# Kernel optimization log

Measured on AMD Instinct MI355X. Metric: run time of the kernel, lower is better.

Reference implementation:

```python
import jax, jax.numpy as jnp
import numpy as np

EPS = 1e-5

def conv1x1(x, W, b):
    # x: [B,C,H,W], W: [O,C], b: [O] -- a 1x1 conv is a per-pixel matmul
    return jnp.einsum('bchw,oc->bohw', x, W) + b[None, :, None, None]

def mean_variance_norm(feat):
    # torch .var(dim=2) is unbiased (ddof=1)
    m = feat.mean(axis=(2, 3), keepdims=True)
    v = feat.var(axis=(2, 3), ddof=1, keepdims=True)
    return (feat - m) / jnp.sqrt(v + EPS)

def setup_inputs() -> dict:
    key = jax.random.key(0)
    ks = jax.random.split(key, 10)
    B, C, H, W = 4, 256, 64, 64
    sc = 1.0 / np.sqrt(C)
    return {
        'content': jax.random.normal(ks[0], (B, C, H, W), jnp.float32),
        'style': jax.random.normal(ks[1], (B, C, H, W), jnp.float32),
        'content_key': jax.random.normal(ks[2], (B, C, H, W), jnp.float32),
        'style_key': jax.random.normal(ks[3], (B, C, H, W), jnp.float32),
        'Wf': jax.random.normal(ks[4], (C, C), jnp.float32) * sc,
        'bf': jnp.zeros((C,), jnp.float32),
        'Wg': jax.random.normal(ks[5], (C, C), jnp.float32) * sc,
        'bg': jnp.zeros((C,), jnp.float32),
        'Wh': jax.random.normal(ks[6], (C, C), jnp.float32) * sc,
        'bh': jnp.zeros((C,), jnp.float32),
    }

def reference(content, style, content_key, style_key, Wf, bf, Wg, bg, Wh, bh):
    Fq = conv1x1(content_key, Wf, bf)   # [B,Ck,H,W]
    G = conv1x1(style_key, Wg, bg)      # [B,Ck,Hs,Ws]
    Hv = conv1x1(style, Wh, bh)         # [B,C,Hs,Ws]
    b, _, h, w = Fq.shape
    _, C, hs, ws = Hv.shape
    N, M = h * w, hs * ws
    q = Fq.reshape(b, -1, N).transpose(0, 2, 1)   # [B,N,Ck]
    k = G.reshape(b, -1, M)                        # [B,Ck,M]
    style_flat = Hv.reshape(b, C, M).transpose(0, 2, 1)  # [B,M,C]
    # masks are all-ones -> attn_mask all zeros -> no masking (faithful to None path)
    S = jax.nn.softmax(jnp.einsum('bnc,bcm->bnm', q, k), axis=-1)  # [B,N,M]
    mean = jnp.einsum('bnm,bmc->bnc', S, style_flat)               # [B,N,C]
    std = jnp.sqrt(jax.nn.relu(
        jnp.einsum('bnm,bmc->bnc', S, style_flat * style_flat) - mean * mean))
    mean = mean.reshape(b, h, w, C).transpose(0, 3, 1, 2)  # [B,C,H,W]
    std = std.reshape(b, h, w, C).transpose(0, 3, 1, 2)
    return std * mean_variance_norm(content) + mean
```

## Files before the change

### kernel.cpp

```cpp
#include <hip/hip_runtime.h>


typedef unsigned int u32;
typedef unsigned short u16;
typedef _Float16 f16x8 __attribute__((ext_vector_type(8)));
typedef float f32x4 __attribute__((ext_vector_type(4)));
typedef float f32x16 __attribute__((ext_vector_type(16)));

#define L2E 1.44269504088896340736f
#define MFMA(a, b, c) __builtin_amdgcn_mfma_f32_16x16x32_f16(a, b, c, 0, 0, 0)
#define MFMA32(a, b, c) __builtin_amdgcn_mfma_f32_32x32x16_f16(a, b, c, 0, 0, 0)
#define EXP2(x) __builtin_amdgcn_exp2f(x)

__device__ __forceinline__ u16 h_bits(_Float16 h) { return __builtin_bit_cast(u16, h); }
__device__ __forceinline__ u16 f2h(float f) { return h_bits((_Float16)f); }

__device__ __forceinline__ f16x8 ldh8(const u16* p) {
    uint4 v = *(const uint4*)p;
    return __builtin_bit_cast(f16x8, v);
}

__global__ void k_stats(const float* __restrict__ content,
                        float* __restrict__ cm, float* __restrict__ cr) {
    int blk = blockIdx.x;
    const float* p = content + (size_t)blk * 4096;
    int t = threadIdx.x;
    float s = 0.f, ss = 0.f;
    for (int i = 0; i < 4; i++) {
        float4 v = *(const float4*)(p + (i * 256 + t) * 4);
        s  += (v.x + v.y) + (v.z + v.w);
        ss += (v.x * v.x + v.y * v.y) + (v.z * v.z + v.w * v.w);
    }
    for (int d = 32; d >= 1; d >>= 1) { s += __shfl_xor(s, d); ss += __shfl_xor(ss, d); }
    __shared__ __align__(16) float as[4], ass[4];
    int w = t >> 6;
    if ((t & 63) == 0) { as[w] = s; ass[w] = ss; }
    __syncthreads();
    if (t == 0) {
        s  = (as[0] + as[1]) + (as[2] + as[3]);
        ss = (ass[0] + ass[1]) + (ass[2] + ass[3]);
        float mean = s * (1.0f / 4096.0f);
        float var = (ss - s * mean) * (1.0f / 4095.0f);
        cm[blk] = mean;
        cr[blk] = rsqrtf(var + 1e-5f);
    }
}

__global__ void k_prep(const float* __restrict__ style, const float* __restrict__ ckey,
                       const float* __restrict__ skey,
                       const float* __restrict__ Wf, const float* __restrict__ Wg,
                       const float* __restrict__ Wh,
                       u16* __restrict__ X1, u16* __restrict__ X2, u16* __restrict__ Cc,
                       u16* __restrict__ Wb) {
    int z = blockIdx.z, t = threadIdx.x;
    if (z >= 12) {
        if (blockIdx.y != 0) return;
        int m = z - 12;
        const float* src = (m == 0) ? Wf : ((m == 1) ? Wg : Wh);
        u16* dst = Wb + m * 65536;
        int i = (blockIdx.x * 256 + t) * 4;
        float4 v = *(const float4*)(src + i);
        ushort4 o;
        o.x = f2h(v.x); o.y = f2h(v.y); o.z = f2h(v.z); o.w = f2h(v.w);
        *(ushort4*)(dst + i) = o;
        return;
    }
    int tensor = z >> 2, b = z & 3;
    const float* src = ((tensor == 0) ? style : ((tensor == 1) ? ckey : skey))
                       + (size_t)b * 256 * 4096;
    u16* dst = ((tensor == 0) ? X1 : ((tensor == 1) ? X2 : Cc)) + (size_t)b * 4096 * 256;
    int c0 = blockIdx.y * 64, t0 = blockIdx.x * 64;
    __shared__ __align__(16) float ls[64][65];
    int tr = t >> 4, tc = t & 15;
    for (int i = 0; i < 4; i++) {
        int c_off = i * 16 + tr;
        float4 v = *(const float4*)(src + (size_t)(c0 + c_off) * 4096 + t0 + tc * 4);
        ls[tc * 4 + 0][c_off] = v.x;
        ls[tc * 4 + 1][c_off] = v.y;
        ls[tc * 4 + 2][c_off] = v.z;
        ls[tc * 4 + 3][c_off] = v.w;
    }
    __syncthreads();
    for (int i = 0; i < 4; i++) {
        int tokrow = i * 16 + tr;
        ushort4 o;
        o.x = f2h(ls[tokrow][tc * 4 + 0]);
        o.y = f2h(ls[tokrow][tc * 4 + 1]);
        o.z = f2h(ls[tokrow][tc * 4 + 2]);
        o.w = f2h(ls[tokrow][tc * 4 + 3]);
        *(ushort4*)(dst + (size_t)(t0 + tokrow) * 256 + c0 + tc * 4) = o;
    }
}

__launch_bounds__(256, 2)
__global__ void k_gemm(const u16* X1, const u16* X2, u16* Cc,
                       u16* A, u16* Bv, const u16* __restrict__ Wb,
                       const float* __restrict__ bfp, const float* __restrict__ bgp,
                       const float* __restrict__ bhp) {
    int mode = blockIdx.z, b = blockIdx.y, tok0 = blockIdx.x * 128;
    const u16* X = ((mode == 0) ? X2 : ((mode == 1) ? (const u16*)Cc : X1))
                   + (size_t)b * 4096 * 256;
    const u16* W = Wb + mode * 65536;
    const float* bias = (mode == 0) ? bfp : ((mode == 1) ? bgp : bhp);
    __shared__ __align__(16) u16 wt[256 * 40];
    int t = threadIdx.x, w = t >> 6, lane = t & 63, ln = lane & 15, quad = lane >> 4;

    f32x4 acc[8][4];
    for (int i = 0; i < 8; i++)
        for (int j = 0; j < 4; j++) acc[i][j] = f32x4{0.f, 0.f, 0.f, 0.f};

    for (int ks = 0; ks < 8; ks++) {
        {
            const u16* wr = W + t * 256 + ks * 32;
            uint4 w0 = *(const uint4*)(wr + 0);
            uint4 w1 = *(const uint4*)(wr + 8);
            uint4 w2 = *(const uint4*)(wr + 16);
            uint4 w3 = *(const uint4*)(wr + 24);
            *(uint4*)(wt + t * 40 + 0)  = w0;
            *(uint4*)(wt + t * 40 + 8)  = w1;
            *(uint4*)(wt + t * 40 + 16) = w2;
            *(uint4*)(wt + t * 40 + 24) = w3;
        }
        __syncthreads();
        f16x8 wf[4];
        #pragma unroll
        for (int ct = 0; ct < 4; ct++)
            wf[ct] = ldh8(wt + (w * 64 + ct * 16 + ln) * 40 + quad * 8);
        #pragma unroll
        for (int rt = 0; rt < 8; rt++) {
            f16x8 xf = ldh8(X + (size_t)(tok0 + rt * 16 + ln) * 256 + ks * 32 + quad * 8);
            if (mode < 2) {
                #pragma unroll
                for (int ct = 0; ct < 4; ct++) acc[rt][ct] = MFMA(xf, wf[ct], acc[rt][ct]);
            } else {
                #pragma unroll
                for (int ct = 0; ct < 4; ct++) acc[rt][ct] = MFMA(wf[ct], xf, acc[rt][ct]);
            }
        }
        __syncthreads();
    }

    if (mode < 2) {
        u16* O = ((mode == 0) ? A : Cc) + (size_t)b * 4096 * 256;
        float bv[4];
        #pragma unroll
        for (int ct = 0; ct < 4; ct++) bv[ct] = bias[w * 64 + ct * 16 + ln];
        #pragma unroll
        for (int rt = 0; rt < 8; rt++)
            #pragma unroll
            for (int ct = 0; ct < 4; ct++)
                #pragma unroll
                for (int r = 0; r < 4; r++) {
                    int tok = tok0 + rt * 16 + quad * 4 + r;
                    int o = w * 64 + ct * 16 + ln;
                    O[(size_t)tok * 256 + o] = f2h(acc[rt][ct][r] + bv[ct]);
                }
    } else {
        u16* OV = Bv + (size_t)b * 256 * 4096;
        #pragma unroll
        for (int ct = 0; ct < 4; ct++)
            #pragma unroll
            for (int r = 0; r < 4; r++) {
                int o = w * 64 + ct * 16 + quad * 4 + r;
                float bb = bias[o];
                #pragma unroll
                for (int rt = 0; rt < 8; rt++) {
                    int tok = tok0 + rt * 16 + ln;
                    OV[(size_t)o * 4096 + tok] = f2h(acc[rt][ct][r] + bb);
                }
            }
    }
}

__launch_bounds__(256, 2)
__global__ void k_flash(const u16* __restrict__ Qt, const u16* __restrict__ Kt,
                        const u16* __restrict__ Vt,
                        const float* __restrict__ content, const float* __restrict__ cm,
                        const float* __restrict__ cr, float* __restrict__ out) {
    __shared__ __align__(16) char smem[67584];
    u16* Ks = (u16*)smem;
    u16* Vs = (u16*)(smem + 33792);
    int t = threadIdx.x, w = t >> 6, l = t & 63, lq = l & 31, h = l >> 5;
    u16* Psw = (u16*)(smem + 43008) + w * 2304;

    int b = blockIdx.y, q0 = blockIdx.x * 128, coff = blockIdx.z * 64;

    f16x8 qf[16];
    {
        const u16* qp = Qt + ((size_t)b * 4096 + q0 + w * 32 + lq) * 256 + h * 8;
        #pragma unroll
        for (int ks = 0; ks < 16; ks++) qf[ks] = ldh8(qp + ks * 16);
    }

    f32x16 am[2], aq[2];
    #pragma unroll
    for (int i = 0; i < 16; i++) { am[0][i] = 0.f; am[1][i] = 0.f; aq[0][i] = 0.f; aq[1][i] = 0.f; }
    float mrow = -1e30f, lrow = 0.f;

    const u16* Kg = Kt + (size_t)b * 4096 * 256;
    const u16* Vg = Vt + ((size_t)b * 256 + coff) * 4096;

    for (int it = 0; it < 64; it++) {
        int m0 = it * 64;
        #pragma unroll
        for (int i = 0; i < 8; i++) {
            int e = i * 256 + t, row = e >> 5, c16 = e & 31;
            *(uint4*)(Ks + row * 264 + c16 * 8) =
                *(const uint4*)(Kg + (size_t)(m0 + row) * 256 + c16 * 8);
        }
        #pragma unroll
        for (int i = 0; i < 2; i++) {
            int e = i * 256 + t, row = e >> 3, m16 = e & 7;
            *(uint4*)(Vs + row * 72 + m16 * 8) =
                *(const uint4*)(Vg + (size_t)row * 4096 + m0 + m16 * 8);
        }
        __syncthreads();

        f32x16 s0, s1;
        #pragma unroll
        for (int i = 0; i < 16; i++) { s0[i] = 0.f; s1[i] = 0.f; }
        #pragma unroll
        for (int ks = 0; ks < 16; ks++) {
            f16x8 k0 = ldh8(Ks + lq * 264 + ks * 16 + h * 8);
            s0 = MFMA32(k0, qf[ks], s0);
            f16x8 k1 = ldh8(Ks + (32 + lq) * 264 + ks * 16 + h * 8);
            s1 = MFMA32(k1, qf[ks], s1);
        }

        float mt = s0[0];
        #pragma unroll
        for (int r = 1; r < 16; r++) mt = fmaxf(mt, s0[r]);
        #pragma unroll
        for (int r = 0; r < 16; r++) mt = fmaxf(mt, s1[r]);
        mt = fmaxf(mt, __shfl_xor(mt, 32));
        float mn = fmaxf(mrow, mt);
        float al = EXP2((mrow - mn) * L2E);
        mrow = mn;
        float base = mn * L2E;
        float rs = 0.f;
        #pragma unroll
        for (int r = 0; r < 16; r++) {
            float p0 = (float)(_Float16)EXP2(__builtin_fmaf(s0[r], L2E, -base));
            float p1 = (float)(_Float16)EXP2(__builtin_fmaf(s1[r], L2E, -base));
            s0[r] = p0; s1[r] = p1;
            rs += p0 + p1;
        }
        rs += __shfl_xor(rs, 32);
        lrow = lrow * al + rs;

        #pragma unroll
        for (int r = 0; r < 16; r++) {
            float sc = __shfl(al, 8 * (r >> 2) + 4 * h + (r & 3));
            am[0][r] *= sc; am[1][r] *= sc;
            aq[0][r] *= sc; aq[1][r] *= sc;
        }

        #pragma unroll
        for (int mt2 = 0; mt2 < 2; mt2++)
            #pragma unroll
            for (int rq = 0; rq < 4; rq++) {
                float e0 = mt2 ? s1[4 * rq + 0] : s0[4 * rq + 0];
                float e1 = mt2 ? s1[4 * rq + 1] : s0[4 * rq + 1];
                float e2 = mt2 ? s1[4 * rq + 2] : s0[4 * rq + 2];
                float e3 = mt2 ? s1[4 * rq + 3] : s0[4 * rq + 3];
                uint2 pk;
                pk.x = (u32)f2h(e0) | ((u32)f2h(e1) << 16);
                pk.y = (u32)f2h(e2) | ((u32)f2h(e3) << 16);
                *(uint2*)(Psw + lq * 72 + mt2 * 32 + rq * 8 + h * 4) = pk;
            }

        #pragma unroll
        for (int ks = 0; ks < 4; ks++) {
            f16x8 pf = ldh8(Psw + lq * 72 + ks * 16 + h * 8);
            #pragma unroll
            for (int ct = 0; ct < 2; ct++) {
                f16x8 vf = ldh8(Vs + (ct * 32 + lq) * 72 + ks * 16 + h * 8);
                am[ct] = MFMA32(pf, vf, am[ct]);
                f16x8 vh = vf * vf;
                f16x8 vl = __builtin_elementwise_fma(vf, vf, -vh);
                aq[ct] = MFMA32(pf, vh, aq[ct]);
                aq[ct] = MFMA32(pf, vl, aq[ct]);
            }
        }
        __syncthreads();
    }

    float inv = 1.0f / lrow;
    float iv[16];
    #pragma unroll
    for (int r = 0; r < 16; r++) iv[r] = __shfl(inv, (r & 3) + 8 * (r >> 2) + 4 * h);
    float* Ms = (float*)smem;
    float* Ss = (float*)(smem + 33792);
    #pragma unroll
    for (int ct = 0; ct < 2; ct++)
        #pragma unroll
        for (int rq = 0; rq < 4; rq++) {
            f32x4 mv, sv;
            #pragma unroll
            for (int j = 0; j < 4; j++) {
                int r = 4 * rq + j;
                float mean = am[ct][r] * iv[r];
                float ex2 = aq[ct][r] * iv[r];
                float var = ex2 - mean * mean;
                mv[j] = mean;
                sv[j] = sqrtf(fmaxf(var, 0.f));
            }
            int c = ct * 32 + lq;
            int qloc = w * 32 + 8 * rq + 4 * h;
            *(f32x4*)(Ms + c * 132 + qloc) = mv;
            *(f32x4*)(Ss + c * 132 + qloc) = sv;
        }
    __syncthreads();
    #pragma unroll
    for (int pass = 0; pass < 8; pass++) {
        int c = pass * 8 + (t >> 5);
        int qloc = (t & 31) * 4;
        f32x4 mv = *(const f32x4*)(Ms + c * 132 + qloc);
        f32x4 sv = *(const f32x4*)(Ss + c * 132 + qloc);
        int gc = coff + c;
        size_t basei = ((size_t)b * 256 + gc) * 4096 + q0 + qloc;
        float4 cv = *(const float4*)(content + basei);
        float cmv = cm[b * 256 + gc], crv = cr[b * 256 + gc];
        float4 o;
        o.x = sv[0] * ((cv.x - cmv) * crv) + mv[0];
        o.y = sv[1] * ((cv.y - cmv) * crv) + mv[1];
        o.z = sv[2] * ((cv.z - cmv) * crv) + mv[2];
        o.w = sv[3] * ((cv.w - cmv) * crv) + mv[3];
        *(float4*)(out + basei) = o;
    }
}

extern "C" void kernel_launch(void* const* d_in, const int* in_sizes, int n_in,
                              void* d_out, int out_size, void* d_ws, size_t ws_size,
                              hipStream_t stream) {
    const float* content = (const float*)d_in[0];
    const float* style   = (const float*)d_in[1];
    const float* ckey    = (const float*)d_in[2];
    const float* skey    = (const float*)d_in[3];
    const float* Wf      = (const float*)d_in[4];
    const float* bfp     = (const float*)d_in[5];
    const float* Wg      = (const float*)d_in[6];
    const float* bgp     = (const float*)d_in[7];
    const float* Wh      = (const float*)d_in[8];
    const float* bhp     = (const float*)d_in[9];
    float* out = (float*)d_out;
    char* ws = (char*)d_ws;

    float* cm = (float*)(ws + 0);
    float* cr = (float*)(ws + 4096);
    u16*   Wb = (u16*)(ws + 8192);
    u16*   A  = (u16*)(ws + 1048576);
    u16*   Bv = (u16*)(ws + 9437184);
    u16*   Cc = (u16*)(ws + 17825792);
    u16*   X1 = (u16*)d_out;
    u16*   X2 = (u16*)d_out + 4194304;

    k_stats<<<dim3(1024), 256, 0, stream>>>(content, cm, cr);
    k_prep<<<dim3(64, 4, 15), 256, 0, stream>>>(style, ckey, skey, Wf, Wg, Wh,
                                                X1, X2, Cc, Wb);
    k_gemm<<<dim3(32, 4, 3), 256, 0, stream>>>(X1, X2, Cc, A, Bv, Wb, bfp, bgp, bhp);
    k_flash<<<dim3(32, 4, 4), 256, 0, stream>>>(A, Cc, Bv, content, cm, cr, out);
}
```

Measured before the change: 411.0 us.

## Prefetch K/V into registers, keep P in registers via permlane32 swap, lazy rescale

The flash loop now loads the next K/V tile into registers while the current tile is computed, so global latency overlaps compute. The P tile no longer round-trips through shared memory: it is packed to fp16 and rearranged in registers with v_permlane32_swap. Online-softmax rescaling is skipped when the new max exceeds the old by at most 8, and max/sum reductions are tree-shaped. The change also adds s_setprio around the MFMA blocks and a barrier that waits only on LDS. The cost is higher register pressure under launch_bounds(256,2), and the lazy-rescale threshold allows probabilities up to 2^11.5, which may stress fp16 range.

```diff
diff --git a/kernel.cpp b/kernel.cpp
--- a/kernel.cpp
+++ b/kernel.cpp
@@ -6,6 +6,7 @@
 typedef _Float16 f16x8 __attribute__((ext_vector_type(8)));
 typedef float f32x4 __attribute__((ext_vector_type(4)));
 typedef float f32x16 __attribute__((ext_vector_type(16)));
+typedef unsigned int u32x2 __attribute__((ext_vector_type(2)));
 
 #define L2E 1.44269504088896340736f
 #define MFMA(a, b, c) __builtin_amdgcn_mfma_f32_16x16x32_f16(a, b, c, 0, 0, 0)
@@ -14,10 +15,28 @@
 
 __device__ __forceinline__ u16 h_bits(_Float16 h) { return __builtin_bit_cast(u16, h); }
 __device__ __forceinline__ u16 f2h(float f) { return h_bits((_Float16)f); }
+__device__ __forceinline__ u32 pk2(float a, float b) {
+    return (u32)f2h(a) | ((u32)f2h(b) << 16);
+}
 
 __device__ __forceinline__ f16x8 ldh8(const u16* p) {
     uint4 v = *(const uint4*)p;
     return __builtin_bit_cast(f16x8, v);
+}
+
+__device__ __forceinline__ u32x2 pl32_swap(u32 a, u32 b) {
+#if __has_builtin(__builtin_amdgcn_permlane32_swap)
+    return __builtin_amdgcn_permlane32_swap(a, b, false, false);
+#else
+    asm("v_permlane32_swap_b32 %0, %1" : "+v"(a), "+v"(b));
+    u32x2 r; r.x = a; r.y = b; return r;
+#endif
+}
+
+__device__ __forceinline__ void barrier_nv() {
+    asm volatile("s_waitcnt lgkmcnt(0)" ::: "memory");
+    __builtin_amdgcn_s_barrier();
+    asm volatile("" ::: "memory");
 }
 
 __global__ void k_stats(const float* __restrict__ content,
@@ -181,7 +200,6 @@
     u16* Ks = (u16*)smem;
     u16* Vs = (u16*)(smem + 33792);
     int t = threadIdx.x, w = t >> 6, l = t & 63, lq = l & 31, h = l >> 5;
-    u16* Psw = (u16*)(smem + 43008) + w * 2304;
 
     int b = blockIdx.y, q0 = blockIdx.x * 128, coff = blockIdx.z * 64;
 
@@ -200,25 +218,48 @@
     const u16* Kg = Kt + (size_t)b * 4096 * 256;
     const u16* Vg = Vt + ((size_t)b * 256 + coff) * 4096;
 
+    uint4 kr[8], vr[2];
+    #pragma unroll
+    for (int i = 0; i < 8; i++) {
+        int e = i * 256 + t;
+        kr[i] = *(const uint4*)(Kg + (size_t)(e >> 5) * 256 + (e & 31) * 8);
+    }
+    #pragma unroll
+    for (int i = 0; i < 2; i++) {
+        int e = i * 256 + t;
+        vr[i] = *(const uint4*)(Vg + (size_t)(e >> 3) * 4096 + (e & 7) * 8);
+    }
+
     for (int it = 0; it < 64; it++) {
-        int m0 = it * 64;
         #pragma unroll
         for (int i = 0; i < 8; i++) {
-            int e = i * 256 + t, row = e >> 5, c16 = e & 31;
-            *(uint4*)(Ks + row * 264 + c16 * 8) =
-                *(const uint4*)(Kg + (size_t)(m0 + row) * 256 + c16 * 8);
+            int e = i * 256 + t;
+            *(uint4*)(Ks + (e >> 5) * 264 + (e & 31) * 8) = kr[i];
         }
         #pragma unroll
         for (int i = 0; i < 2; i++) {
-            int e = i * 256 + t, row = e >> 3, m16 = e & 7;
-            *(uint4*)(Vs + row * 72 + m16 * 8) =
-                *(const uint4*)(Vg + (size_t)row * 4096 + m0 + m16 * 8);
-        }
-        __syncthreads();
+            int e = i * 256 + t;
+            *(uint4*)(Vs + (e >> 3) * 72 + (e & 7) * 8) = vr[i];
+        }
+        if (it < 63) {
+            int m0n = (it + 1) * 64;
+            #pragma unroll
+            for (int i = 0; i < 8; i++) {
+                int e = i * 256 + t;
+                kr[i] = *(const uint4*)(Kg + (size_t)(m0n + (e >> 5)) * 256 + (e & 31) * 8);
+            }
+            #pragma unroll
+            for (int i = 0; i < 2; i++) {
+                int e = i * 256 + t;
+                vr[i] = *(const uint4*)(Vg + (size_t)(e >> 3) * 4096 + m0n + (e & 7) * 8);
+            }
+        }
+        barrier_nv();
 
         f32x16 s0, s1;
         #pragma unroll
         for (int i = 0; i < 16; i++) { s0[i] = 0.f; s1[i] = 0.f; }
+        __builtin_amdgcn_s_setprio(1);
         #pragma unroll
         for (int ks = 0; ks < 16; ks++) {
             f16x8 k0 = ldh8(Ks + lq * 264 + ks * 16 + h * 8);
@@ -226,52 +267,77 @@
             f16x8 k1 = ldh8(Ks + (32 + lq) * 264 + ks * 16 + h * 8);
             s1 = MFMA32(k1, qf[ks], s1);
         }
-
-        float mt = s0[0];
-        #pragma unroll
-        for (int r = 1; r < 16; r++) mt = fmaxf(mt, s0[r]);
-        #pragma unroll
-        for (int r = 0; r < 16; r++) mt = fmaxf(mt, s1[r]);
-        mt = fmaxf(mt, __shfl_xor(mt, 32));
-        float mn = fmaxf(mrow, mt);
-        float al = EXP2((mrow - mn) * L2E);
-        mrow = mn;
+        __builtin_amdgcn_s_setprio(0);
+
+        float m8[8];
+        #pragma unroll
+        for (int r = 0; r < 8; r++)
+            m8[r] = fmaxf(fmaxf(s0[r], s0[r + 8]), fmaxf(s1[r], s1[r + 8]));
+        #pragma unroll
+        for (int d = 4; d >= 1; d >>= 1)
+            #pragma unroll
+            for (int r = 0; r < d; r++) m8[r] = fmaxf(m8[r], m8[r + d]);
+        float mt = fmaxf(m8[0], __shfl_xor(m8[0], 32));
+
+        float mn, al;
+        bool resc = !__all(mt - mrow <= 8.0f);
+        if (resc) {
+            mn = fmaxf(mrow, mt);
+            al = EXP2((mrow - mn) * L2E);
+            mrow = mn;
+        } else {
+            mn = mrow;
+            al = 1.0f;
+        }
         float base = mn * L2E;
-        float rs = 0.f;
         #pragma unroll
         for (int r = 0; r < 16; r++) {
             float p0 = (float)(_Float16)EXP2(__builtin_fmaf(s0[r], L2E, -base));
             float p1 = (float)(_Float16)EXP2(__builtin_fmaf(s1[r], L2E, -base));
             s0[r] = p0; s1[r] = p1;
-            rs += p0 + p1;
-        }
-        rs += __shfl_xor(rs, 32);
+        }
+        float a8[8];
+        #pragma unroll
+        for (int r = 0; r < 8; r++)
+            a8[r] = (s0[r] + s0[r + 8]) + (s1[r] + s1[r + 8]);
+        #pragma unroll
+        for (int d = 4; d >= 1; d >>= 1)
+            #pragma unroll
+            for (int r = 0; r < d; r++) a8[r] += a8[r + d];
+        float rs = a8[0] + __shfl_xor(a8[0], 32);
         lrow = lrow * al + rs;
 
-        #pragma unroll
-        for (int r = 0; r < 16; r++) {
-            float sc = __shfl(al, 8 * (r >> 2) + 4 * h + (r & 3));
-            am[0][r] *= sc; am[1][r] *= sc;
-            aq[0][r] *= sc; aq[1][r] *= sc;
-        }
-
-        #pragma unroll
-        for (int mt2 = 0; mt2 < 2; mt2++)
-            #pragma unroll
-            for (int rq = 0; rq < 4; rq++) {
-                float e0 = mt2 ? s1[4 * rq + 0] : s0[4 * rq + 0];
-                float e1 = mt2 ? s1[4 * rq + 1] : s0[4 * rq + 1];
-                float e2 = mt2 ? s1[4 * rq + 2] : s0[4 * rq + 2];
-                float e3 = mt2 ? s1[4 * rq + 3] : s0[4 * rq + 3];
-                uint2 pk;
-                pk.x = (u32)f2h(e0) | ((u32)f2h(e1) << 16);
-                pk.y = (u32)f2h(e2) | ((u32)f2h(e3) << 16);
-                *(uint2*)(Psw + lq * 72 + mt2 * 32 + rq * 8 + h * 4) = pk;
-            }
-
+        if (resc) {
+            #pragma unroll
+            for (int r = 0; r < 16; r++) {
+                float sc = __shfl(al, 8 * (r >> 2) + 4 * h + (r & 3));
+                am[0][r] *= sc; am[1][r] *= sc;
+                aq[0][r] *= sc; aq[1][r] *= sc;
+            }
+        }
+
+        f16x8 pfr[4];
+        #pragma unroll
+        for (int mt2 = 0; mt2 < 2; mt2++) {
+            f32x16 sv = mt2 ? s1 : s0;
+            u32 d0 = pk2(sv[0], sv[1]),  d1 = pk2(sv[2], sv[3]);
+            u32 d2 = pk2(sv[4], sv[5]),  d3 = pk2(sv[6], sv[7]);
+            u32 d4 = pk2(sv[8], sv[9]),  d5 = pk2(sv[10], sv[11]);
+            u32 d6 = pk2(sv[12], sv[13]), d7 = pk2(sv[14], sv[15]);
+            u32x2 p02 = pl32_swap(d0, d2);
+            u32x2 p13 = pl32_swap(d1, d3);
+            u32x2 p46 = pl32_swap(d4, d6);
+            u32x2 p57 = pl32_swap(d5, d7);
+            uint4 fa = {p02.x, p13.x, p02.y, p13.y};
+            uint4 fb = {p46.x, p57.x, p46.y, p57.y};
+            pfr[mt2 * 2 + 0] = __builtin_bit_cast(f16x8, fa);
+            pfr[mt2 * 2 + 1] = __builtin_bit_cast(f16x8, fb);
+        }
+
+        __builtin_amdgcn_s_setprio(1);
         #pragma unroll
         for (int ks = 0; ks < 4; ks++) {
-            f16x8 pf = ldh8(Psw + lq * 72 + ks * 16 + h * 8);
+            f16x8 pf = pfr[ks];
             #pragma unroll
             for (int ct = 0; ct < 2; ct++) {
                 f16x8 vf = ldh8(Vs + (ct * 32 + lq) * 72 + ks * 16 + h * 8);
@@ -282,7 +348,8 @@
                 aq[ct] = MFMA32(pf, vl, aq[ct]);
             }
         }
-        __syncthreads();
+        __builtin_amdgcn_s_setprio(0);
+        barrier_nv();
     }
 
     float inv = 1.0f / lrow;
```

Measured after the change: 540.0 us. +31.4%, slower.
